# Kernel optimization log

Measured on AMD Instinct MI355X. Metric: run time of the kernel, lower is better.

The kernel has to match this reference:

```python
import jax, jax.numpy as jnp
import numpy as np

N = 100000  # num nodes
E = 1600000  # num edges
D_IN = 64
D_OUT = 64


def setup_inputs() -> dict:
    key = jax.random.key(0)
    k = jax.random.split(key, 8)
    x = jax.random.normal(k[0], (N, D_IN), dtype=jnp.float32)
    edge_index = jax.random.randint(k[1], (2, E), 0, N, dtype=jnp.int64)
    s1 = 1.0 / np.sqrt(D_IN)
    s2 = 1.0 / np.sqrt(D_OUT)
    W1 = jax.random.uniform(k[2], (D_IN, D_OUT), jnp.float32, -s1, s1)
    b1 = jax.random.uniform(k[3], (D_OUT,), jnp.float32, -s1, s1)
    W2 = jax.random.uniform(k[4], (D_OUT, D_OUT), jnp.float32, -s2, s2)
    b2 = jax.random.uniform(k[5], (D_OUT,), jnp.float32, -s2, s2)
    eps = jnp.asarray(0.0, dtype=jnp.float32)  # learnable (train_eps=True)
    return {"x": x, "edge_index": edge_index, "W1": W1, "b1": b1, "W2": W2, "b2": b2, "eps": eps}


def reference(x, edge_index, W1, b1, W2, b2, eps):
    src, dst = edge_index[0], edge_index[1]
    # sum-aggregate neighbor features: agg[i] = sum_{(j->i)} x[j]
    agg = jax.ops.segment_sum(x[src], dst, num_segments=N)  # [N, D_IN]
    h = (1.0 + eps) * x + agg
    h = jax.nn.relu(h @ W1 + b1)
    return h @ W2 + b2
```

## Files before the change

kernel.cpp:

```cpp
#include <hip/hip_runtime.h>

#define NN 100000
#define NE 1600000
#define D  64
#define NBK 512
#define NPB 196
#define CAP 4096
#define CHUNK 2048
#define NCH ((NE + CHUNK - 1) / CHUNK)
#define CVTB ((NN * D / 4 + 255) / 256)


typedef unsigned short u16;
typedef __attribute__((ext_vector_type(8))) short bf16x8;
typedef __attribute__((ext_vector_type(4))) float f32x4;

__device__ __forceinline__ u16 f32_to_bf16_rn(float f) {
    unsigned u = __float_as_uint(f);
    return (u16)((u + 0x7FFF + ((u >> 16) & 1)) >> 16);
}
__device__ __forceinline__ float bf16_to_f32(u16 h) {
    return __uint_as_float(((unsigned)h) << 16);
}

__global__ __launch_bounds__(256) void bin_cvt_kernel(const float* __restrict__ x,
                                                      u16* __restrict__ xb,
                                                      const int* __restrict__ ei,
                                                      int* __restrict__ cursor,
                                                      int* __restrict__ bins) {
    __shared__ int lc[NBK];
    __shared__ int lbase[NBK];
    const int t = threadIdx.x;

    if (blockIdx.x >= NCH) {
        int i = ((blockIdx.x - NCH) * 256 + t) * 4;
        if (i < NN * D) {
            float4 v = *(const float4*)(x + i);
            ushort4 o;
            o.x = f32_to_bf16_rn(v.x);
            o.y = f32_to_bf16_rn(v.y);
            o.z = f32_to_bf16_rn(v.z);
            o.w = f32_to_bf16_rn(v.w);
            *(ushort4*)(xb + i) = o;
        }
        return;
    }

    const int base = blockIdx.x * CHUNK;

    for (int i = t; i < NBK; i += 256) lc[i] = 0;
    __syncthreads();
    #pragma unroll 4
    for (int j = 0; j < CHUNK / 256; ++j) {
        int e = base + t + j * 256;
        if (e < NE) atomicAdd(&lc[(unsigned)ei[NE + e] / NPB], 1);
    }
    __syncthreads();
    for (int i = t; i < NBK; i += 256) {
        int c = lc[i];
        lbase[i] = c ? atomicAdd(&cursor[i], c) : 0;
        lc[i] = 0;
    }
    __syncthreads();
    #pragma unroll 4
    for (int j = 0; j < CHUNK / 256; ++j) {
        int e = base + t + j * 256;
        if (e < NE) {
            int src = ei[e];
            int dst = ei[NE + e];
            int b   = (unsigned)dst / NPB;
            int loc = dst - b * NPB;
            int o   = atomicAdd(&lc[b], 1);
            int pos = lbase[b] + o;
            if (pos < CAP)
                bins[b * CAP + pos] = (loc << 17) | src;
        }
    }
}

__global__ __launch_bounds__(1024) void agg_kernel(const float* __restrict__ x,
                                                   const u16* __restrict__ xb,
                                                   const float* __restrict__ eps,
                                                   const int* __restrict__ cursor,
                                                   const int* __restrict__ bins,
                                                   float* __restrict__ out) {
    __shared__ int sorted[CAP];
    __shared__ int tmp[256];
    __shared__ int off[256];
    __shared__ int cur[256];
    const int b    = blockIdx.x;
    const int t    = threadIdx.x;
    const int lane = t & 63;
    const int w    = t >> 6;
    const int base = b * CAP;
    const int n    = min(cursor[b], CAP);
    const float e1 = 1.0f + *eps;

    if (t < 256) tmp[t] = 0;
    __syncthreads();
    for (int i = t; i < n; i += 1024)
        atomicAdd(&tmp[bins[base + i] >> 17], 1);
    __syncthreads();
    int v = (t < 256) ? tmp[t] : 0;
    for (int o = 1; o < 256; o <<= 1) {
        int u = (t < 256 && t >= o) ? tmp[t - o] : 0;
        __syncthreads();
        if (t < 256) tmp[t] += u;
        __syncthreads();
    }
    if (t < 256) { off[t] = tmp[t] - v; cur[t] = tmp[t] - v; }
    __syncthreads();
    for (int i = t; i < n; i += 1024) {
        int pk  = bins[base + i];
        int pos = atomicAdd(&cur[pk >> 17], 1);
        sorted[pos] = pk & 0x1FFFF;
    }
    __syncthreads();

    #pragma unroll
    for (int j = 0; j < 13; ++j) {
        int r = w + 16 * j;
        if (r < NPB) {
            int node = b * NPB + r;
            if (node < NN) {
                float a = e1 * x[node * D + lane];
                int p  = off[r];
                int pe = off[r + 1];
                for (; p + 8 <= pe; p += 8) {
                    int i0 = sorted[p],     i1 = sorted[p + 1];
                    int i2 = sorted[p + 2], i3 = sorted[p + 3];
                    int i4 = sorted[p + 4], i5 = sorted[p + 5];
                    int i6 = sorted[p + 6], i7 = sorted[p + 7];
                    float v0 = bf16_to_f32(xb[i0 * D + lane]);
                    float v1 = bf16_to_f32(xb[i1 * D + lane]);
                    float v2 = bf16_to_f32(xb[i2 * D + lane]);
                    float v3 = bf16_to_f32(xb[i3 * D + lane]);
                    float v4 = bf16_to_f32(xb[i4 * D + lane]);
                    float v5 = bf16_to_f32(xb[i5 * D + lane]);
                    float v6 = bf16_to_f32(xb[i6 * D + lane]);
                    float v7 = bf16_to_f32(xb[i7 * D + lane]);
                    a += ((v0 + v1) + (v2 + v3)) + ((v4 + v5) + (v6 + v7));
                }
                for (; p + 4 <= pe; p += 4) {
                    int i0 = sorted[p],     i1 = sorted[p + 1];
                    int i2 = sorted[p + 2], i3 = sorted[p + 3];
                    float v0 = bf16_to_f32(xb[i0 * D + lane]);
                    float v1 = bf16_to_f32(xb[i1 * D + lane]);
                    float v2 = bf16_to_f32(xb[i2 * D + lane]);
                    float v3 = bf16_to_f32(xb[i3 * D + lane]);
                    a += (v0 + v1) + (v2 + v3);
                }
                for (; p < pe; ++p) a += bf16_to_f32(xb[sorted[p] * D + lane]);
                out[node * D + lane] = a;
            }
        }
    }
}

__global__ __launch_bounds__(256, 2) void mlp_mfma_kernel(
        float* __restrict__ h,
        const float* __restrict__ W1, const float* __restrict__ b1,
        const float* __restrict__ W2, const float* __restrict__ b2) {
    __shared__ u16 lds[4][16 * 72];
    const int lane = threadIdx.x & 63;
    const int wv   = threadIdx.x >> 6;
    const int m    = lane & 15;
    const int q    = lane >> 4;
    u16* tile = &lds[wv][0];

    bf16x8 wb1[4][2], wb2[4][2];
    #pragma unroll
    for (int t = 0; t < 4; ++t)
        #pragma unroll
        for (int s = 0; s < 2; ++s) {
            bf16x8 f1, f2;
            #pragma unroll
            for (int j = 0; j < 8; ++j) {
                int k = s * 32 + q * 8 + j;
                int nn = t * 16 + m;
                f1[j] = (short)f32_to_bf16_rn(W1[k * D + nn]);
                f2[j] = (short)f32_to_bf16_rn(W2[k * D + nn]);
            }
            wb1[t][s] = f1;
            wb2[t][s] = f2;
        }
    float bias1[4], bias2[4];
    #pragma unroll
    for (int t = 0; t < 4; ++t) {
        bias1[t] = b1[t * 16 + m];
        bias2[t] = b2[t * 16 + m];
    }

    const int wave = blockIdx.x * 4 + wv;
    const int nw   = gridDim.x * 4;
    for (int ti = wave; ti < NN / 16; ti += nw) {
        const int rowbase = ti * 16;

        bf16x8 a1f[2];
        #pragma unroll
        for (int s = 0; s < 2; ++s) {
            const float* p = h + (rowbase + m) * D + s * 32 + q * 8;
            float4 v0 = *(const float4*)p;
            float4 v1 = *(const float4*)(p + 4);
            bf16x8 f;
            f[0] = (short)f32_to_bf16_rn(v0.x);
            f[1] = (short)f32_to_bf16_rn(v0.y);
            f[2] = (short)f32_to_bf16_rn(v0.z);
            f[3] = (short)f32_to_bf16_rn(v0.w);
            f[4] = (short)f32_to_bf16_rn(v1.x);
            f[5] = (short)f32_to_bf16_rn(v1.y);
            f[6] = (short)f32_to_bf16_rn(v1.z);
            f[7] = (short)f32_to_bf16_rn(v1.w);
            a1f[s] = f;
        }

        #pragma unroll
        for (int t = 0; t < 4; ++t) {
            f32x4 c = {0.f, 0.f, 0.f, 0.f};
            c = __builtin_amdgcn_mfma_f32_16x16x32_bf16(a1f[0], wb1[t][0], c, 0, 0, 0);
            c = __builtin_amdgcn_mfma_f32_16x16x32_bf16(a1f[1], wb1[t][1], c, 0, 0, 0);
            #pragma unroll
            for (int r = 0; r < 4; ++r) {
                float vv = fmaxf(c[r] + bias1[t], 0.0f);
                tile[(q * 4 + r) * 72 + t * 16 + m] = f32_to_bf16_rn(vv);
            }
        }

        bf16x8 a2f[2];
        #pragma unroll
        for (int s = 0; s < 2; ++s)
            a2f[s] = *(const bf16x8*)&tile[m * 72 + s * 32 + q * 8];

        #pragma unroll
        for (int t = 0; t < 4; ++t) {
            f32x4 c = {0.f, 0.f, 0.f, 0.f};
            c = __builtin_amdgcn_mfma_f32_16x16x32_bf16(a2f[0], wb2[t][0], c, 0, 0, 0);
            c = __builtin_amdgcn_mfma_f32_16x16x32_bf16(a2f[1], wb2[t][1], c, 0, 0, 0);
            #pragma unroll
            for (int r = 0; r < 4; ++r)
                h[(rowbase + q * 4 + r) * D + t * 16 + m] = c[r] + bias2[t];
        }
    }
}

extern "C" void kernel_launch(void* const* d_in, const int* in_sizes, int n_in,
                              void* d_out, int out_size, void* d_ws, size_t ws_size,
                              hipStream_t stream) {
    const float* x   = (const float*)d_in[0];
    const int*   ei  = (const int*)d_in[1];
    const float* W1  = (const float*)d_in[2];
    const float* b1  = (const float*)d_in[3];
    const float* W2  = (const float*)d_in[4];
    const float* b2  = (const float*)d_in[5];
    const float* eps = (const float*)d_in[6];
    float*       out = (float*)d_out;

    int* cursor = (int*)d_ws;
    int* bins   = cursor + NBK;
    u16* xb     = (u16*)(bins + NBK * CAP);

    hipMemsetAsync(cursor, 0, NBK * sizeof(int), stream);
    bin_cvt_kernel<<<NCH + CVTB, 256, 0, stream>>>(x, xb, ei, cursor, bins);
    agg_kernel<<<NBK, 1024, 0, stream>>>(x, xb, eps, cursor, bins, out);
    mlp_mfma_kernel<<<1024, 256, 0, stream>>>(out, W1, b1, W2, b2);
}
```

Baseline: 181.1 us.

## Replicate bin cursors and gather bf16 rows with vector loads per quarter-wave

Each destination bucket's global cursor is split into 8 replicas keyed by block index, so fewer binning blocks contend on the same atomic. The aggregation gather now has each 16-lane quarter of a wave load a whole neighbor row as 8-byte vectors, covering four edges per instruction, and combines the partial sums with cross-lane shuffles. The MLP grid also grows to 1563 blocks. In exchange, each replica caps at 512 edges, which raises the risk of silently dropping edges on skewed inputs, and the shuffle reduction adds work per node.

```diff
diff --git a/kernel.cpp b/kernel.cpp
--- a/kernel.cpp
+++ b/kernel.cpp
@@ -5,7 +5,8 @@
 #define D  64
 #define NBK 512
 #define NPB 196
-#define CAP 4096
+#define RPL 8
+#define CAPR 512
 #define CHUNK 2048
 #define NCH ((NE + CHUNK - 1) / CHUNK)
 #define CVTB ((NN * D / 4 + 255) / 256)
@@ -19,8 +20,11 @@
     unsigned u = __float_as_uint(f);
     return (u16)((u + 0x7FFF + ((u >> 16) & 1)) >> 16);
 }
-__device__ __forceinline__ float bf16_to_f32(u16 h) {
-    return __uint_as_float(((unsigned)h) << 16);
+__device__ __forceinline__ float bflo(unsigned w) {
+    return __uint_as_float(w << 16);
+}
+__device__ __forceinline__ float bfhi(unsigned w) {
+    return __uint_as_float(w & 0xFFFF0000u);
 }
 
 __global__ __launch_bounds__(256) void bin_cvt_kernel(const float* __restrict__ x,
@@ -47,6 +51,7 @@
     }
 
     const int base = blockIdx.x * CHUNK;
+    const int rep  = blockIdx.x & (RPL - 1);
 
     for (int i = t; i < NBK; i += 256) lc[i] = 0;
     __syncthreads();
@@ -58,7 +63,7 @@
     __syncthreads();
     for (int i = t; i < NBK; i += 256) {
         int c = lc[i];
-        lbase[i] = c ? atomicAdd(&cursor[i], c) : 0;
+        lbase[i] = c ? atomicAdd(&cursor[rep * NBK + i], c) : 0;
         lc[i] = 0;
     }
     __syncthreads();
@@ -72,8 +77,8 @@
             int loc = dst - b * NPB;
             int o   = atomicAdd(&lc[b], 1);
             int pos = lbase[b] + o;
-            if (pos < CAP)
-                bins[b * CAP + pos] = (loc << 17) | src;
+            if (pos < CAPR)
+                bins[(b * RPL + rep) * CAPR + pos] = (loc << 17) | src;
         }
     }
 }
@@ -84,7 +89,7 @@
                                                    const int* __restrict__ cursor,
                                                    const int* __restrict__ bins,
                                                    float* __restrict__ out) {
-    __shared__ int sorted[CAP];
+    __shared__ int sorted[RPL * CAPR];
     __shared__ int tmp[256];
     __shared__ int off[256];
     __shared__ int cur[256];
@@ -92,14 +97,19 @@
     const int t    = threadIdx.x;
     const int lane = t & 63;
     const int w    = t >> 6;
-    const int base = b * CAP;
-    const int n    = min(cursor[b], CAP);
     const float e1 = 1.0f + *eps;
 
     if (t < 256) tmp[t] = 0;
     __syncthreads();
-    for (int i = t; i < n; i += 1024)
-        atomicAdd(&tmp[bins[base + i] >> 17], 1);
+    int nrep[RPL];
+    #pragma unroll
+    for (int r = 0; r < RPL; ++r) nrep[r] = min(cursor[r * NBK + b], CAPR);
+    #pragma unroll
+    for (int r = 0; r < RPL; ++r) {
+        const int rb = (b * RPL + r) * CAPR;
+        for (int i = t; i < nrep[r]; i += 1024)
+            atomicAdd(&tmp[bins[rb + i] >> 17], 1);
+    }
     __syncthreads();
     int v = (t < 256) ? tmp[t] : 0;
     for (int o = 1; o < 256; o <<= 1) {
@@ -110,48 +120,68 @@
     }
     if (t < 256) { off[t] = tmp[t] - v; cur[t] = tmp[t] - v; }
     __syncthreads();
-    for (int i = t; i < n; i += 1024) {
-        int pk  = bins[base + i];
-        int pos = atomicAdd(&cur[pk >> 17], 1);
-        sorted[pos] = pk & 0x1FFFF;
-    }
-    __syncthreads();
-
+    #pragma unroll
+    for (int r = 0; r < RPL; ++r) {
+        const int rb = (b * RPL + r) * CAPR;
+        for (int i = t; i < nrep[r]; i += 1024) {
+            int pk  = bins[rb + i];
+            int pos = atomicAdd(&cur[pk >> 17], 1);
+            sorted[pos] = pk & 0x1FFFF;
+        }
+    }
+    __syncthreads();
+
+    const int g = lane >> 4;
+    const int c = lane & 15;
     #pragma unroll
     for (int j = 0; j < 13; ++j) {
         int r = w + 16 * j;
         if (r < NPB) {
             int node = b * NPB + r;
             if (node < NN) {
-                float a = e1 * x[node * D + lane];
+                float4 a;
+                if (g == 0) {
+                    float4 xv = *(const float4*)(x + node * D + 4 * c);
+                    a.x = e1 * xv.x; a.y = e1 * xv.y;
+                    a.z = e1 * xv.z; a.w = e1 * xv.w;
+                } else {
+                    a.x = a.y = a.z = a.w = 0.f;
+                }
                 int p  = off[r];
                 int pe = off[r + 1];
                 for (; p + 8 <= pe; p += 8) {
-                    int i0 = sorted[p],     i1 = sorted[p + 1];
-                    int i2 = sorted[p + 2], i3 = sorted[p + 3];
-                    int i4 = sorted[p + 4], i5 = sorted[p + 5];
-                    int i6 = sorted[p + 6], i7 = sorted[p + 7];
-                    float v0 = bf16_to_f32(xb[i0 * D + lane]);
-                    float v1 = bf16_to_f32(xb[i1 * D + lane]);
-                    float v2 = bf16_to_f32(xb[i2 * D + lane]);
-                    float v3 = bf16_to_f32(xb[i3 * D + lane]);
-                    float v4 = bf16_to_f32(xb[i4 * D + lane]);
-                    float v5 = bf16_to_f32(xb[i5 * D + lane]);
-                    float v6 = bf16_to_f32(xb[i6 * D + lane]);
-                    float v7 = bf16_to_f32(xb[i7 * D + lane]);
-                    a += ((v0 + v1) + (v2 + v3)) + ((v4 + v5) + (v6 + v7));
+                    int e0 = sorted[p + g];
+                    int e1i = sorted[p + 4 + g];
+                    uint2 v0 = *(const uint2*)(xb + e0 * D + 4 * c);
+                    uint2 v1 = *(const uint2*)(xb + e1i * D + 4 * c);
+                    a.x += bflo(v0.x) + bflo(v1.x);
+                    a.y += bfhi(v0.x) + bfhi(v1.x);
+                    a.z += bflo(v0.y) + bflo(v1.y);
+                    a.w += bfhi(v0.y) + bfhi(v1.y);
                 }
                 for (; p + 4 <= pe; p += 4) {
-                    int i0 = sorted[p],     i1 = sorted[p + 1];
-                    int i2 = sorted[p + 2], i3 = sorted[p + 3];
-                    float v0 = bf16_to_f32(xb[i0 * D + lane]);
-                    float v1 = bf16_to_f32(xb[i1 * D + lane]);
-                    float v2 = bf16_to_f32(xb[i2 * D + lane]);
-                    float v3 = bf16_to_f32(xb[i3 * D + lane]);
-                    a += (v0 + v1) + (v2 + v3);
-                }
-                for (; p < pe; ++p) a += bf16_to_f32(xb[sorted[p] * D + lane]);
-                out[node * D + lane] = a;
+                    int e0 = sorted[p + g];
+                    uint2 v0 = *(const uint2*)(xb + e0 * D + 4 * c);
+                    a.x += bflo(v0.x);
+                    a.y += bfhi(v0.x);
+                    a.z += bflo(v0.y);
+                    a.w += bfhi(v0.y);
+                }
+                if (p < pe) {
+                    bool ok = (p + g) < pe;
+                    int e0 = sorted[ok ? p + g : p];
+                    uint2 v0 = *(const uint2*)(xb + e0 * D + 4 * c);
+                    a.x += ok ? bflo(v0.x) : 0.f;
+                    a.y += ok ? bfhi(v0.x) : 0.f;
+                    a.z += ok ? bflo(v0.y) : 0.f;
+                    a.w += ok ? bfhi(v0.y) : 0.f;
+                }
+                a.x += __shfl_xor(a.x, 16); a.x += __shfl_xor(a.x, 32);
+                a.y += __shfl_xor(a.y, 16); a.y += __shfl_xor(a.y, 32);
+                a.z += __shfl_xor(a.z, 16); a.z += __shfl_xor(a.z, 32);
+                a.w += __shfl_xor(a.w, 16); a.w += __shfl_xor(a.w, 32);
+                if (g == 0)
+                    *(float4*)(out + node * D + 4 * c) = a;
             }
         }
     }
@@ -216,12 +246,12 @@
 
         #pragma unroll
         for (int t = 0; t < 4; ++t) {
-            f32x4 c = {0.f, 0.f, 0.f, 0.f};
-            c = __builtin_amdgcn_mfma_f32_16x16x32_bf16(a1f[0], wb1[t][0], c, 0, 0, 0);
-            c = __builtin_amdgcn_mfma_f32_16x16x32_bf16(a1f[1], wb1[t][1], c, 0, 0, 0);
+            f32x4 cc = {0.f, 0.f, 0.f, 0.f};
+            cc = __builtin_amdgcn_mfma_f32_16x16x32_bf16(a1f[0], wb1[t][0], cc, 0, 0, 0);
+            cc = __builtin_amdgcn_mfma_f32_16x16x32_bf16(a1f[1], wb1[t][1], cc, 0, 0, 0);
             #pragma unroll
             for (int r = 0; r < 4; ++r) {
-                float vv = fmaxf(c[r] + bias1[t], 0.0f);
+                float vv = fmaxf(cc[r] + bias1[t], 0.0f);
                 tile[(q * 4 + r) * 72 + t * 16 + m] = f32_to_bf16_rn(vv);
             }
         }
@@ -233,12 +263,12 @@
 
         #pragma unroll
         for (int t = 0; t < 4; ++t) {
-            f32x4 c = {0.f, 0.f, 0.f, 0.f};
-            c = __builtin_amdgcn_mfma_f32_16x16x32_bf16(a2f[0], wb2[t][0], c, 0, 0, 0);
-            c = __builtin_amdgcn_mfma_f32_16x16x32_bf16(a2f[1], wb2[t][1], c, 0, 0, 0);
+            f32x4 cc = {0.f, 0.f, 0.f, 0.f};
+            cc = __builtin_amdgcn_mfma_f32_16x16x32_bf16(a2f[0], wb2[t][0], cc, 0, 0, 0);
+            cc = __builtin_amdgcn_mfma_f32_16x16x32_bf16(a2f[1], wb2[t][1], cc, 0, 0, 0);
             #pragma unroll
             for (int r = 0; r < 4; ++r)
-                h[(rowbase + q * 4 + r) * D + t * 16 + m] = c[r] + bias2[t];
+                h[(rowbase + q * 4 + r) * D + t * 16 + m] = cc[r] + bias2[t];
         }
     }
 }
@@ -256,11 +286,11 @@
     float*       out = (float*)d_out;
 
     int* cursor = (int*)d_ws;
-    int* bins   = cursor + NBK;
-    u16* xb     = (u16*)(bins + NBK * CAP);
-
-    hipMemsetAsync(cursor, 0, NBK * sizeof(int), stream);
+    int* bins   = cursor + RPL * NBK;
+    u16* xb     = (u16*)(bins + NBK * RPL * CAPR);
+
+    hipMemsetAsync(cursor, 0, RPL * NBK * sizeof(int), stream);
     bin_cvt_kernel<<<NCH + CVTB, 256, 0, stream>>>(x, xb, ei, cursor, bins);
     agg_kernel<<<NBK, 1024, 0, stream>>>(x, xb, eps, cursor, bins, out);
-    mlp_mfma_kernel<<<1024, 256, 0, stream>>>(out, W1, b1, W2, b2);
-}
+    mlp_mfma_kernel<<<1563, 256, 0, stream>>>(out, W1, b1, W2, b2);
+}
```

Measured after the change: 164.0 us. 1.1x faster.
